# Kernel optimization log

Hardware: AMD Instinct MI355X
Metric: run time of the kernel (lower is better)

Reference implementation:

```python
import jax, jax.numpy as jnp
from jax import lax
import numpy as np

B, T, U, V = 4, 300, 64, 1024
FEAT, H, L = 80, 512, 3            # encoder: 3-layer bidirectional LSTM
HD = 512                           # decoder hidden (1 layer)
ENC_OUT = DEC_OUT = 512
INNER = 512
DMAX = max(FEAT, 2 * H)            # padded input dim for stacked encoder weights
NEG = -1e30


def setup_inputs() -> dict:
    key = jax.random.key(0)
    ks = jax.random.split(key, 20)
    s = 1.0 / np.sqrt(H)
    u = lambda k, shp: jax.random.uniform(k, shp, jnp.float32, -s, s)
    inputs = jax.random.normal(ks[0], (B, T, FEAT), jnp.float32)
    inputs_length = jax.random.randint(ks[1], (B,), T // 2, T + 1, jnp.int32)
    targets = jax.random.randint(ks[2], (B, U), 1, V, jnp.int32)
    targets_length = jax.random.randint(ks[3], (B,), U // 2, U + 1, jnp.int32)
    enc_Wih = u(ks[4], (L, 2, 4 * H, DMAX))   # layer0 uses first FEAT cols
    enc_Whh = u(ks[5], (L, 2, 4 * H, H))
    enc_b = u(ks[6], (L, 2, 4 * H))           # b_ih + b_hh fused
    enc_proj_W = u(ks[7], (ENC_OUT, 2 * H))
    enc_proj_b = u(ks[8], (ENC_OUT,))
    dec_emb = u(ks[9], (V, HD)).at[0].set(0.0)  # padding_idx=0
    dec_Wih = u(ks[10], (4 * HD, HD))
    dec_Whh = u(ks[11], (4 * HD, HD))
    dec_b = u(ks[12], (4 * HD,))
    dec_proj_W = u(ks[13], (DEC_OUT, HD))
    dec_proj_b = u(ks[14], (DEC_OUT,))
    j_fwd_W = u(ks[15], (INNER, ENC_OUT + DEC_OUT))
    j_fwd_b = u(ks[16], (INNER,))
    j_proj_W = u(ks[17], (V, INNER))
    j_proj_b = u(ks[18], (V,))
    return dict(inputs=inputs, inputs_length=inputs_length, targets=targets,
                targets_length=targets_length, enc_Wih=enc_Wih, enc_Whh=enc_Whh,
                enc_b=enc_b, enc_proj_W=enc_proj_W, enc_proj_b=enc_proj_b,
                dec_emb=dec_emb, dec_Wih=dec_Wih, dec_Whh=dec_Whh, dec_b=dec_b,
                dec_proj_W=dec_proj_W, dec_proj_b=dec_proj_b, j_fwd_W=j_fwd_W,
                j_fwd_b=j_fwd_b, j_proj_W=j_proj_W, j_proj_b=j_proj_b)


def lstm_layer(x, Wih, Whh, b):
    # x: [B, T, Din]; torch gate order (i, f, g, o)
    Bb = x.shape[0]
    Hh = Whh.shape[1]
    xg = jnp.einsum('btd,gd->btg', x, Wih) + b  # precompute input projections

    def step(carry, xt):
        h, c = carry
        g = xt + h @ Whh.T
        i, f, gg, o = jnp.split(g, 4, axis=-1)
        c = jax.nn.sigmoid(f) * c + jax.nn.sigmoid(i) * jnp.tanh(gg)
        h = jax.nn.sigmoid(o) * jnp.tanh(c)
        return (h, c), h

    z = jnp.zeros((Bb, Hh), x.dtype)
    _, hs = lax.scan(step, (z, z), xg.transpose(1, 0, 2))
    return hs.transpose(1, 0, 2)


def reverse_padded(x, lengths):
    # reverse each sequence within its valid length (packed-sequence semantics)
    t = jnp.arange(x.shape[1])
    idx = jnp.where(t[None] < lengths[:, None], lengths[:, None] - 1 - t[None], t[None])
    return jnp.take_along_axis(x, idx[:, :, None], axis=1)


def rnnt_loss(log_probs, targets, T_len, U_len):
    # log_probs: [B, T, U+1, V], blank = 0
    Bb, Tt, U1, _ = log_probs.shape
    Uu = U1 - 1
    blank = log_probs[..., 0]                                   # [B,T,U+1]
    idx = jnp.broadcast_to(targets[:, None, :, None], (Bb, Tt, Uu, 1))
    lab = jnp.take_along_axis(log_probs[:, :, :Uu, :], idx, axis=3)[..., 0]  # [B,T,U]

    def row_update(a, c):
        # solves x[u] = logaddexp(a[u], x[u-1] + c[u-1]) via log-space cumsum
        C = jnp.concatenate([jnp.zeros((Bb, 1), a.dtype), jnp.cumsum(c, axis=1)], axis=1)
        return C + lax.cumlogsumexp(a - C, axis=1)

    a0 = jnp.full((Bb, U1), NEG, log_probs.dtype).at[:, 0].set(0.0)
    alpha0 = row_update(a0, lab[:, 0])

    def step(alpha_prev, xs):
        bl_prev, lab_t = xs
        alpha = row_update(alpha_prev + bl_prev, lab_t)
        return alpha, alpha

    xs = (blank[:, :-1].transpose(1, 0, 2), lab[:, 1:].transpose(1, 0, 2))
    _, alphas = lax.scan(step, alpha0, xs)                      # [T-1,B,U+1]
    alphas = jnp.concatenate([alpha0[None], alphas], axis=0)    # [T,B,U+1]
    b_idx = jnp.arange(Bb)
    ll = alphas[T_len - 1, b_idx, U_len] + blank[b_idx, T_len - 1, U_len]
    return -jnp.mean(ll)


def reference(inputs, inputs_length, targets, targets_length, enc_Wih, enc_Whh,
              enc_b, enc_proj_W, enc_proj_b, dec_emb, dec_Wih, dec_Whh, dec_b,
              dec_proj_W, dec_proj_b, j_fwd_W, j_fwd_b, j_proj_W, j_proj_b):
    # ---- encoder: stacked bi-LSTM + projection ----
    mask = (jnp.arange(T)[None] < inputs_length[:, None])[..., None].astype(inputs.dtype)
    x = inputs
    for l in range(L):
        Din = x.shape[-1]
        fwd = lstm_layer(x, enc_Wih[l, 0, :, :Din], enc_Whh[l, 0], enc_b[l, 0])
        bwd = reverse_padded(
            lstm_layer(reverse_padded(x, inputs_length), enc_Wih[l, 1, :, :Din],
                       enc_Whh[l, 1], enc_b[l, 1]), inputs_length)
        x = jnp.concatenate([fwd, bwd], axis=-1) * mask
    enc = jnp.einsum('bth,oh->bto', x, enc_proj_W) + enc_proj_b  # [B,T,ENC_OUT]

    # ---- decoder: blank-prepended targets -> embed -> LSTM -> projection ----
    dec_in = jnp.pad(targets, ((0, 0), (1, 0)))                  # [B,U+1]
    demb = dec_emb[dec_in]
    dmask = (jnp.arange(U + 1)[None] < (targets_length + 1)[:, None])[..., None].astype(demb.dtype)
    dh = lstm_layer(demb, dec_Wih, dec_Whh, dec_b) * dmask
    dec = jnp.einsum('buh,oh->buo', dh, dec_proj_W) + dec_proj_b  # [B,U+1,DEC_OUT]

    # ---- joint: broadcast T x (U+1), split concat-matmul into two matmuls ----
    We, Wd = j_fwd_W[:, :ENC_OUT], j_fwd_W[:, ENC_OUT:]
    hj = jnp.tanh(jnp.einsum('bto,io->bti', enc, We)[:, :, None, :]
                  + jnp.einsum('buo,io->bui', dec, Wd)[:, None, :, :] + j_fwd_b)
    logits = jnp.einsum('btui,vi->btuv', hj, j_proj_W) + j_proj_b  # [B,T,U+1,V]
    log_probs = jax.nn.log_softmax(logits, axis=-1)

    return rnnt_loss(log_probs, targets, inputs_length, targets_length)
```

## Files before the change

kernel.cpp:

```cpp
#include <hip/hip_runtime.h>
#include <hip/hip_bf16.h>

#define B_ 4
#define T_ 300
#define U_ 64
#define U1_ 65
#define V_ 1024
#define H_ 512
#define G4_ 2048
#define NW_ 32
#define RPB_ (T_ * U1_)
#define NTILE_ 305
#define RPAD_ 19520
#define FASTK_ 128

typedef __hip_bfloat16 bf16;
typedef unsigned long long u64;
typedef __attribute__((ext_vector_type(8))) short short8;
typedef __attribute__((ext_vector_type(4))) float floatx4;
typedef __attribute__((ext_vector_type(4))) unsigned int uintx4;

__device__ __forceinline__ float b2f(bf16 x) { return __bfloat162float(x); }
__device__ __forceinline__ bf16 f2b(float x) { return __float2bfloat16(x); }
__device__ __forceinline__ short bf16bits(float x) {
  bf16 h = __float2bfloat16(x);
  return *reinterpret_cast<short*>(&h);
}
__device__ __forceinline__ short8 pack8(float4 a, float4 b) {
  short8 p;
  p[0] = bf16bits(a.x); p[1] = bf16bits(a.y); p[2] = bf16bits(a.z); p[3] = bf16bits(a.w);
  p[4] = bf16bits(b.x); p[5] = bf16bits(b.y); p[6] = bf16bits(b.z); p[7] = bf16bits(b.w);
  return p;
}
__device__ __forceinline__ float sigm_(float x) { return 1.f / (1.f + __expf(-x)); }
__device__ __forceinline__ float tanh_(float x) { return 1.f - 2.f / (1.f + __expf(2.f * x)); }
__device__ __forceinline__ float lae_(float x, float y) {
  float m = fmaxf(x, y);
  float n = fminf(x, y);
  return m + __logf(1.f + __expf(n - m));
}

__device__ __forceinline__ void poll4x4(const u64* a0, bool slow,
                                        uintx4& q0, uintx4& q1,
                                        uintx4& q2, uintx4& q3) {
  const u64* a1 = a0 + 512;
  const u64* a2 = a0 + 1024;
  const u64* a3 = a0 + 1536;
  if (!slow) {
    asm volatile(
        "global_load_dwordx4 %0, %4, off sc0\n\t"
        "global_load_dwordx4 %1, %5, off sc0\n\t"
        "global_load_dwordx4 %2, %6, off sc0\n\t"
        "global_load_dwordx4 %3, %7, off sc0\n\t"
        "s_waitcnt vmcnt(0)"
        : "=&v"(q0), "=&v"(q1), "=&v"(q2), "=&v"(q3)
        : "v"(a0), "v"(a1), "v"(a2), "v"(a3)
        : "memory");
  } else {
    asm volatile(
        "global_load_dwordx4 %0, %4, off sc0 sc1\n\t"
        "global_load_dwordx4 %1, %5, off sc0 sc1\n\t"
        "global_load_dwordx4 %2, %6, off sc0 sc1\n\t"
        "global_load_dwordx4 %3, %7, off sc0 sc1\n\t"
        "s_waitcnt vmcnt(0)"
        : "=&v"(q0), "=&v"(q1), "=&v"(q2), "=&v"(q3)
        : "v"(a0), "v"(a1), "v"(a2), "v"(a3)
        : "memory");
  }
}

__global__ void zero_hpk_kernel(u64* __restrict__ a, u64* __restrict__ b) {
  int i = blockIdx.x * 256 + threadIdx.x;
  if (i < 7 * 4096) { a[i] = 0ull; b[i] = 0ull; }
}

__global__ void prep_kernel(const float* __restrict__ in, bf16* __restrict__ x0) {
  int i = blockIdx.x * 256 + threadIdx.x;
  if (i < B_ * T_ * 128) {
    int k = i & 127;
    int row = i >> 7;
    float v = (k < 80) ? in[row * 80 + k] : 0.f;
    x0[(size_t)row * 1024 + k] = f2b(v);
  }
}

__global__ void embed_kernel(const float* __restrict__ emb, const int* __restrict__ tgt,
                             bf16* __restrict__ demb) {
  int i = blockIdx.x * 256 + threadIdx.x;
  if (i >= B_ * U1_ * 512) return;
  int k = i & 511;
  int bu = i >> 9;
  int u = bu % U1_, b = bu / U1_;
  int id = (u == 0) ? 0 : tgt[b * U_ + u - 1];
  demb[i] = f2b(emb[(size_t)id * 512 + k]);
}

__global__ __launch_bounds__(256) void gemm_kernel(
    const bf16* __restrict__ A, int lda,
    const float* __restrict__ W, int ldw,
    const float* __restrict__ bias,
    void* __restrict__ Cout, int out_f32, int ldc,
    int M, int K) {
  __shared__ __align__(16) bf16 As[64][72];
  __shared__ __align__(16) bf16 Bs[64][72];
  int m0 = blockIdx.x * 64, n0 = blockIdx.y * 64;
  int tid = threadIdx.x, w = tid >> 6, l = tid & 63;
  int l4 = l & 15, lq = l >> 4;
  floatx4 acc[4];
#pragma unroll
  for (int nt = 0; nt < 4; ++nt) acc[nt] = (floatx4){0.f, 0.f, 0.f, 0.f};
  for (int k0 = 0; k0 < K; k0 += 64) {
    __syncthreads();
#pragma unroll
    for (int q = 0; q < 2; ++q) {
      int cc = tid + q * 256;
      int r = cc >> 3, kc = (cc & 7) * 8;
      short8 va = {0, 0, 0, 0, 0, 0, 0, 0};
      int gm = m0 + r;
      if (gm < M) va = *(const short8*)(A + (size_t)gm * lda + k0 + kc);
      *(short8*)(&As[r][kc]) = va;
      const float* wp = W + (size_t)(n0 + r) * ldw + k0 + kc;
      float4 w0 = *(const float4*)(wp);
      float4 w1 = *(const float4*)(wp + 4);
      *(short8*)(&Bs[r][kc]) = pack8(w0, w1);
    }
    __syncthreads();
#pragma unroll
    for (int kk = 0; kk < 64; kk += 32) {
      short8 a = *(const short8*)(&As[w * 16 + l4][kk + lq * 8]);
#pragma unroll
      for (int nt = 0; nt < 4; ++nt) {
        short8 bb = *(const short8*)(&Bs[nt * 16 + l4][kk + lq * 8]);
        acc[nt] = __builtin_amdgcn_mfma_f32_16x16x32_bf16(a, bb, acc[nt], 0, 0, 0);
      }
    }
  }
#pragma unroll
  for (int nt = 0; nt < 4; ++nt) {
    int col = n0 + nt * 16 + l4;
    float bv = bias ? bias[col] : 0.f;
#pragma unroll
    for (int r = 0; r < 4; ++r) {
      int row = m0 + w * 16 + lq * 4 + r;
      if (row < M) {
        float v = acc[nt][r] + bv;
        if (out_f32) ((float*)Cout)[(size_t)row * ldc + col] = v;
        else ((bf16*)Cout)[(size_t)row * ldc + col] = f2b(v);
      }
    }
  }
}

__global__ __launch_bounds__(256, 1) void scan_kernel(
    int ndir,
    const float* __restrict__ xg,
    const float* __restrict__ whh,
    const int* __restrict__ len_raw, int len_add,
    int Tmax, int bwd_mask,
    bf16* __restrict__ out, int out_stride,
    int dec_d,
    const float* __restrict__ xg2, const float* __restrict__ whh2,
    const int* __restrict__ len_raw2, int len_add2,
    int Tmax2, bf16* __restrict__ out2, int out_stride2,
    u64* __restrict__ hpkS, u64* __restrict__ hpkF) {
  int d = blockIdx.x, w = blockIdx.y;
  if (d >= ndir) return;
  int tid = threadIdx.x;
  bool isdec = (d == dec_d);
  const float* xg_d = isdec ? xg2 : xg + (size_t)d * B_ * Tmax * G4_;
  const float* whh_d = isdec ? whh2 : whh + (size_t)d * G4_ * H_;
  const int* lens = isdec ? len_raw2 : len_raw;
  int ladd = isdec ? len_add2 : len_add;
  int tmax = isdec ? Tmax2 : Tmax;
  bf16* outp = isdec ? out2 : out;
  int ostride = isdec ? out_stride2 : out_stride;
  int ocol = isdec ? 0 : d * H_;
  bool bwd = isdec ? false : ((bwd_mask >> d) & 1);
  u64* hpS = hpkS + (size_t)d * 4096;
  u64* hpF = hpkF + (size_t)d * 4096;

  int sub = tid >> 6;
  int l = tid & 63;
  int col = l & 15;
  int lq = l >> 4;
  int gate = col & 3;
  int dloc = col >> 2;
  int dim = w * 16 + sub * 4 + dloc;
  int grow = gate * H_ + dim;
  int sb = l & 12;

  __shared__ int len_s[4];
  __shared__ __align__(16) bf16 h_lds[2][16][512];

  if (tid < 4) len_s[tid] = lens[tid] + ladd;
  {
    unsigned* hz = (unsigned*)&h_lds[0][0][0];
#pragma unroll
    for (int i = 0; i < 32; ++i) hz[tid + i * 256] = 0u;
  }

  short8 bfr[16];
  {
    const float* wp = whh_d + (size_t)grow * H_ + lq * 8;
#pragma unroll
    for (int ks2 = 0; ks2 < 16; ++ks2) {
      float4 w0 = *(const float4*)(wp + ks2 * 32);
      float4 w1 = *(const float4*)(wp + ks2 * 32 + 4);
      bfr[ks2] = pack8(w0, w1);
    }
  }
  __syncthreads();
  int smax = max(max(len_s[0], len_s[1]), max(len_s[2], len_s[3]));

  int D0 = sub * 128 + 2 * l;
  float cst = 0.f;
  char* hbase = (char*)&h_lds[0][0][0];
  unsigned rsw = (unsigned)((l & 7) << 4);
  unsigned rbyte = (unsigned)((l & 15) * 1024 + lq * 16);

  bool slowp = false;

  float xv[4];
  if (l < 16) {
#pragma unroll
    for (int b = 0; b < 4; ++b) {
      int lb = len_s[b];
      int rt = bwd ? (lb - 1) : 0;
      xv[b] = xg_d[((size_t)b * tmax + rt) * G4_ + grow];
    }
  }

  for (int s = 0; s < smax; ++s) {
    int p = s & 1;
    char* pl = hbase + p * 16384;
    if (s > 0) {
      unsigned ss = (unsigned)s;
      const u64* srcS = hpS + ((s - 1) & 1) * 2048 + D0;
      const u64* srcF = hpF + ((s - 1) & 1) * 2048 + D0;
      uintx4 q0, q1, q2, q3;
      int it = 0;
      for (;;) {
        poll4x4(slowp ? srcS : srcF, slowp, q0, q1, q2, q3);
        bool ok = (q0[0] == ss) & (q0[2] == ss) & (q1[0] == ss) & (q1[2] == ss) &
                  (q2[0] == ss) & (q2[2] == ss) & (q3[0] == ss) & (q3[2] == ss);
        if (__all(ok)) break;
        if (!slowp && ++it > FASTK_) slowp = true;
      }
      unsigned cb = (unsigned)(D0 * 2);
      unsigned pay0[4] = {q0[1], q1[1], q2[1], q3[1]};
      unsigned pay1[4] = {q0[3], q1[3], q2[3], q3[3]};
#pragma unroll
      for (int b = 0; b < 4; ++b) {
        float f0 = __uint_as_float(pay0[b]);
        float f1 = __uint_as_float(pay1[b]);
        bf16 h0 = f2b(f0), h1 = f2b(f1);
        float r0 = f0 - b2f(h0), r1 = f1 - b2f(h1);
        bf16 e0 = f2b(r0), e1 = f2b(r1);
        unsigned hi = (unsigned)*(unsigned short*)&h0 |
                      ((unsigned)*(unsigned short*)&h1 << 16);
        unsigned lo = (unsigned)*(unsigned short*)&e0 |
                      ((unsigned)*(unsigned short*)&e1 << 16);
        *(unsigned*)(pl + (((unsigned)(b * 1024) + cb) ^ (unsigned)(b << 4))) = hi;
        *(unsigned*)(pl + (((unsigned)((b + 4) * 1024) + cb) ^ (unsigned)((b + 4) << 4))) = lo;
      }
    }
    float xvn[4];
    if (l < 16) {
      int sn = s + 1;
#pragma unroll
      for (int b = 0; b < 4; ++b) {
        int lb = len_s[b];
        int rt = bwd ? (lb - 1 - sn) : sn;
        if (sn >= lb) rt = 0;
        xvn[b] = xg_d[((size_t)b * tmax + rt) * G4_ + grow];
      }
    }
    __syncthreads();
    floatx4 accA = (floatx4){0.f, 0.f, 0.f, 0.f};
    floatx4 accB = (floatx4){0.f, 0.f, 0.f, 0.f};
#pragma unroll
    for (int k2 = 0; k2 < 16; k2 += 2) {
      short8 a0 = *(const short8*)(pl + ((rbyte + (unsigned)(k2 * 64)) ^ rsw));
      short8 a1 = *(const short8*)(pl + ((rbyte + (unsigned)((k2 + 1) * 64)) ^ rsw));
      accA = __builtin_amdgcn_mfma_f32_16x16x32_bf16(a0, bfr[k2], accA, 0, 0, 0);
      accB = __builtin_amdgcn_mfma_f32_16x16x32_bf16(a1, bfr[k2 + 1], accB, 0, 0, 0);
    }
    floatx4 acc = accA + accB;
    float hout = 0.f;
#pragma unroll
    for (int r = 0; r < 4; ++r) {
      float v2 = acc[r] + __shfl(acc[r], col + 16, 64);
      if (l < 16) v2 += xv[r];
      float gi = __shfl(v2, sb + 0, 64);
      float gf = __shfl(v2, sb + 1, 64);
      float gg = __shfl(v2, sb + 2, 64);
      float go = __shfl(v2, sb + 3, 64);
      if (l < 16 && (l & 3) == r && s < len_s[r]) {
        cst = sigm_(gf) * cst + sigm_(gi) * tanh_(gg);
        hout = sigm_(go) * tanh_(cst);
      }
    }
    if (l < 16) {
      int b = l & 3;
      u64 pkt = ((u64)__float_as_uint(hout) << 32) | (unsigned)(s + 1);
      u64* paF = hpF + p * 2048 + b * 512 + dim;
      u64* paS = hpS + p * 2048 + b * 512 + dim;
      asm volatile("global_store_dwordx2 %0, %1, off sc0" ::"v"(paF), "v"(pkt)
                   : "memory");
      asm volatile("global_store_dwordx2 %0, %1, off sc0 sc1" ::"v"(paS), "v"(pkt)
                   : "memory");
      if (s < len_s[b]) {
        int t = bwd ? (len_s[b] - 1 - s) : s;
        outp[((size_t)b * tmax + t) * ostride + ocol + dim] = f2b(hout);
      }
    }
#pragma unroll
    for (int b = 0; b < 4; ++b) xv[b] = xvn[b];
  }
}

__global__ __launch_bounds__(256) void joint_kernel(
    const float* __restrict__ ea, const float* __restrict__ da,
    const float* __restrict__ Wp, const float* __restrict__ pb,
    const int* __restrict__ targets,
    float* __restrict__ blankraw, float* __restrict__ labraw,
    float* __restrict__ jstats) {
  __shared__ __align__(16) bf16 As[64][72];
  __shared__ __align__(16) bf16 Bs[256][72];
  __shared__ float bias_s[256];
  __shared__ int tgt_s[64];
  __shared__ float pstat[64][2][2];

  int tid = threadIdx.x;
  int tile = blockIdx.x, cb = blockIdx.y, b = blockIdx.z;
  int r0 = tile * 64;

  bias_s[tid & 255] = pb[cb * 256 + (tid & 255)];
  if (tid < 64) {
    int r = r0 + tid;
    int u = r % U1_;
    tgt_s[tid] = (r < RPB_ && u < U_) ? targets[b * U_ + u] : -1;
  }
  int si = tid >> 2;
  int sseg = (tid & 3) * 16;
  int sr = r0 + si;
  bool svalid = sr < RPB_;
  int st = svalid ? sr / U1_ : 0;
  int su = svalid ? sr % U1_ : 0;
  const float* ep = ea + ((size_t)(b * T_ + st)) * 512 + sseg;
  const float* dp = da + ((size_t)(b * U1_ + su)) * 512 + sseg;

  int wid = tid >> 6, l = tid & 63;
  int wm = wid >> 1, wn = wid & 1;
  int l4 = l & 15, lq = l >> 4;

  floatx4 acc[2][8];
#pragma unroll
  for (int ms = 0; ms < 2; ++ms)
#pragma unroll
    for (int nt = 0; nt < 8; ++nt) acc[ms][nt] = (floatx4){0.f, 0.f, 0.f, 0.f};

  for (int k0 = 0; k0 < 512; k0 += 64) {
    __syncthreads();
    {
      const float* e = ep + k0;
      const float* d = dp + k0;
#pragma unroll
      for (int h = 0; h < 2; ++h) {
        float4 e0 = *(const float4*)(e + h * 8);
        float4 e1 = *(const float4*)(e + h * 8 + 4);
        float4 d0 = *(const float4*)(d + h * 8);
        float4 d1 = *(const float4*)(d + h * 8 + 4);
        short8 pk = {0, 0, 0, 0, 0, 0, 0, 0};
        if (svalid) {
          pk[0] = bf16bits(tanh_(e0.x + d0.x));
          pk[1] = bf16bits(tanh_(e0.y + d0.y));
          pk[2] = bf16bits(tanh_(e0.z + d0.z));
          pk[3] = bf16bits(tanh_(e0.w + d0.w));
          pk[4] = bf16bits(tanh_(e1.x + d1.x));
          pk[5] = bf16bits(tanh_(e1.y + d1.y));
          pk[6] = bf16bits(tanh_(e1.z + d1.z));
          pk[7] = bf16bits(tanh_(e1.w + d1.w));
        }
        *(short8*)(&As[si][sseg + h * 8]) = pk;
      }
    }
#pragma unroll
    for (int q = 0; q < 8; ++q) {
      int cc = tid + q * 256;
      int r = cc >> 3, kc = (cc & 7) * 8;
      const float* wp = Wp + (size_t)(cb * 256 + r) * 512 + k0 + kc;
      float4 w0 = *(const float4*)(wp);
      float4 w1 = *(const float4*)(wp + 4);
      *(short8*)(&Bs[r][kc]) = pack8(w0, w1);
    }
    __syncthreads();
#pragma unroll
    for (int kk = 0; kk < 64; kk += 32) {
      short8 af[2], bf8[8];
#pragma unroll
      for (int ms = 0; ms < 2; ++ms)
        af[ms] = *(const short8*)(&As[wm * 32 + ms * 16 + l4][kk + lq * 8]);
#pragma unroll
      for (int nt = 0; nt < 8; ++nt)
        bf8[nt] = *(const short8*)(&Bs[wn * 128 + nt * 16 + l4][kk + lq * 8]);
#pragma unroll
      for (int ms = 0; ms < 2; ++ms)
#pragma unroll
        for (int nt = 0; nt < 8; ++nt)
          acc[ms][nt] = __builtin_amdgcn_mfma_f32_16x16x32_bf16(af[ms], bf8[nt], acc[ms][nt], 0, 0, 0);
    }
  }
#pragma unroll
  for (int ms = 0; ms < 2; ++ms) {
#pragma unroll
    for (int r = 0; r < 4; ++r) {
      int i = wm * 32 + ms * 16 + lq * 4 + r;
      int grow = r0 + i;
      bool valid = grow < RPB_;
      int tg = tgt_s[i];
      float v[8];
      float mx = -1e30f;
#pragma unroll
      for (int nt = 0; nt < 8; ++nt) {
        int colc = wn * 128 + nt * 16 + l4;
        float x = acc[ms][nt][r] + bias_s[colc];
        v[nt] = x;
        mx = fmaxf(mx, x);
        int gcol = cb * 256 + colc;
        if (valid) {
          if (gcol == 0) blankraw[(size_t)b * RPB_ + grow] = x;
          if (gcol == tg) labraw[(size_t)b * RPB_ + grow] = x;
        }
      }
#pragma unroll
      for (int dd = 1; dd < 16; dd <<= 1) mx = fmaxf(mx, __shfl_xor(mx, dd, 64));
      float se = 0.f;
#pragma unroll
      for (int nt = 0; nt < 8; ++nt) se += __expf(v[nt] - mx);
#pragma unroll
      for (int dd = 1; dd < 16; dd <<= 1) se += __shfl_xor(se, dd, 64);
      if (l4 == 0) { pstat[i][wn][0] = mx; pstat[i][wn][1] = se; }
    }
  }
  __syncthreads();
  if (tid < 64) {
    float ma = pstat[tid][0][0], sa = pstat[tid][0][1];
    float mb = pstat[tid][1][0], sb = pstat[tid][1][1];
    float mc = fmaxf(ma, mb);
    float sc = sa * __expf(ma - mc) + sb * __expf(mb - mc);
    size_t o = (((size_t)b * RPAD_ + r0 + tid) * 4 + cb) * 2;
    jstats[o] = mc;
    jstats[o + 1] = sc;
  }
}

__global__ void finalize_kernel(const float* __restrict__ jstats,
                                float* __restrict__ blank, float* __restrict__ lab) {
  int g = blockIdx.x * 256 + threadIdx.x;
  if (g >= B_ * RPB_) return;
  int b = g / RPB_, r = g % RPB_;
  const float* st = jstats + ((size_t)b * RPAD_ + r) * 8;
  float M = fmaxf(fmaxf(st[0], st[2]), fmaxf(st[4], st[6]));
  float s = st[1] * __expf(st[0] - M) + st[3] * __expf(st[2] - M) +
            st[5] * __expf(st[4] - M) + st[7] * __expf(st[6] - M);
  float lse = M + __logf(s);
  blank[g] -= lse;
  if ((r % U1_) < U_) lab[g] -= lse;
}

__global__ void loss_kernel(const float* __restrict__ blank, const float* __restrict__ lab,
                            const int* __restrict__ Tl, const int* __restrict__ Ul,
                            float* __restrict__ outp) {
  int b = threadIdx.x >> 6;
  int l = threadIdx.x & 63;
  int TL = Tl[b], UL = Ul[b];
  float alpha_l = 0.f, alpha0 = 0.f;
  for (int t = 0; t < TL; ++t) {
    float a_u0, a_l1;
    if (t == 0) { a_u0 = 0.f; a_l1 = -1e30f; }
    else {
      const float* bl = blank + ((size_t)b * T_ + (t - 1)) * U1_;
      a_u0 = alpha0 + bl[0];
      a_l1 = alpha_l + bl[l + 1];
    }
    const float* lb = lab + ((size_t)b * T_ + t) * U1_;
    float C = lb[l];
#pragma unroll
    for (int dd = 1; dd < 64; dd <<= 1) {
      float o = __shfl_up(C, dd, 64);
      if (l >= dd) C += o;
    }
    float S = a_l1 - C;
#pragma unroll
    for (int dd = 1; dd < 64; dd <<= 1) {
      float o = __shfl_up(S, dd, 64);
      if (l >= dd) S = lae_(S, o);
    }
    alpha_l = C + lae_(a_u0, S);
    alpha0 = a_u0;
  }
  float av = (UL == 0) ? alpha0 : __shfl(alpha_l, UL - 1, 64);
  float ll = av + blank[((size_t)b * T_ + (TL - 1)) * U1_ + UL];
  __shared__ float lls[4];
  if (l == 0) lls[b] = ll;
  __syncthreads();
  if (threadIdx.x == 0) outp[0] = -0.25f * (lls[0] + lls[1] + lls[2] + lls[3]);
}

static constexpr size_t OFF_XG = 0;
static constexpr size_t OFF_XA = OFF_XG + (size_t)2 * B_ * T_ * G4_ * 4;
static constexpr size_t OFF_XB = OFF_XA + (size_t)B_ * T_ * 1024 * 2;
static constexpr size_t OFF_ENC = OFF_XB + (size_t)B_ * T_ * 1024 * 2;
static constexpr size_t OFF_EA = OFF_ENC + (size_t)B_ * T_ * 512 * 2;
static constexpr size_t OFF_DEMB = OFF_EA + (size_t)B_ * T_ * 512 * 4;
static constexpr size_t OFF_DXG = OFF_DEMB + (size_t)B_ * U1_ * 512 * 2;
static constexpr size_t OFF_DH = OFF_DXG + (size_t)B_ * U1_ * G4_ * 4;
static constexpr size_t OFF_DEC = OFF_DH + (size_t)B_ * U1_ * 512 * 2;
static constexpr size_t OFF_DA = OFF_DEC + (size_t)B_ * U1_ * 512 * 2;
static constexpr size_t OFF_BL = OFF_DA + (size_t)B_ * U1_ * 512 * 4;
static constexpr size_t OFF_LAB = OFF_BL + (size_t)B_ * T_ * U1_ * 4;
static constexpr size_t OFF_HPK = OFF_LAB + (size_t)B_ * T_ * U1_ * 4;
static constexpr size_t OFF_JST = OFF_HPK + (size_t)7 * 4096 * 8;
static constexpr size_t OFF_FPK = OFF_JST + (size_t)B_ * RPAD_ * 4 * 2 * 4;

extern "C" void kernel_launch(void* const* d_in, const int* in_sizes, int n_in,
                              void* d_out, int out_size, void* d_ws, size_t ws_size,
                              hipStream_t stream) {
  (void)in_sizes; (void)n_in; (void)out_size; (void)ws_size;
  const float* inputs = (const float*)d_in[0];
  const int* inputs_length = (const int*)d_in[1];
  const int* targets = (const int*)d_in[2];
  const int* targets_length = (const int*)d_in[3];
  const float* enc_Wih = (const float*)d_in[4];
  const float* enc_Whh = (const float*)d_in[5];
  const float* enc_b = (const float*)d_in[6];
  const float* enc_proj_W = (const float*)d_in[7];
  const float* enc_proj_b = (const float*)d_in[8];
  const float* dec_emb = (const float*)d_in[9];
  const float* dec_Wih = (const float*)d_in[10];
  const float* dec_Whh = (const float*)d_in[11];
  const float* dec_b = (const float*)d_in[12];
  const float* dec_proj_W = (const float*)d_in[13];
  const float* dec_proj_b = (const float*)d_in[14];
  const float* j_fwd_W = (const float*)d_in[15];
  const float* j_fwd_b = (const float*)d_in[16];
  const float* j_proj_W = (const float*)d_in[17];
  const float* j_proj_b = (const float*)d_in[18];

  char* ws = (char*)d_ws;
  float* xg = (float*)(ws + OFF_XG);
  bf16* xa = (bf16*)(ws + OFF_XA);
  bf16* xb = (bf16*)(ws + OFF_XB);
  bf16* encb = (bf16*)(ws + OFF_ENC);
  float* eab = (float*)(ws + OFF_EA);
  bf16* demb = (bf16*)(ws + OFF_DEMB);
  float* dxg = (float*)(ws + OFF_DXG);
  bf16* dh = (bf16*)(ws + OFF_DH);
  bf16* decb = (bf16*)(ws + OFF_DEC);
  float* dab = (float*)(ws + OFF_DA);
  float* blank = (float*)(ws + OFF_BL);
  float* lab = (float*)(ws + OFF_LAB);
  u64* hpkS = (u64*)(ws + OFF_HPK);
  u64* hpkF = (u64*)(ws + OFF_FPK);
  float* jstats = (float*)(ws + OFF_JST);

  zero_hpk_kernel<<<112, 256, 0, stream>>>(hpkS, hpkF);
  prep_kernel<<<600, 256, 0, stream>>>(inputs, xa);
  embed_kernel<<<520, 256, 0, stream>>>(dec_emb, targets, demb);

  gemm_kernel<<<dim3(5, 32), 256, 0, stream>>>(demb, 512, dec_Wih, 512, dec_b,
                                               dxg, 1, G4_, B_ * U1_, 512);
  for (int dd = 0; dd < 2; ++dd) {
    gemm_kernel<<<dim3(19, 32), 256, 0, stream>>>(
        xa, 1024, enc_Wih + (size_t)dd * G4_ * 1024, 1024, enc_b + (size_t)dd * G4_,
        xg + (size_t)dd * B_ * T_ * G4_, 1, G4_, B_ * T_, 128);
  }
  scan_kernel<<<dim3(8, NW_), 256, 0, stream>>>(
      3, xg, enc_Whh, inputs_length, 0, T_, 2, xb, 1024,
      2, dxg, dec_Whh, targets_length, 1, U1_, dh, 512,
      hpkS, hpkF);

  gemm_kernel<<<dim3(5, 8), 256, 0, stream>>>(dh, 512, dec_proj_W, 512, dec_proj_b,
                                              decb, 0, 512, B_ * U1_, 512);
  gemm_kernel<<<dim3(5, 8), 256, 0, stream>>>(decb, 512, j_fwd_W + 512, 1024, j_fwd_b,
                                              dab, 1, 512, B_ * U1_, 512);

  bf16* xcur = xb;
  for (int lyr = 1; lyr < 3; ++lyr) {
    bf16* xnext = (xcur == xa) ? xb : xa;
    for (int dd = 0; dd < 2; ++dd) {
      gemm_kernel<<<dim3(19, 32), 256, 0, stream>>>(
          xcur, 1024,
          enc_Wih + (size_t)(lyr * 2 + dd) * G4_ * 1024, 1024,
          enc_b + (size_t)(lyr * 2 + dd) * G4_,
          xg + (size_t)dd * B_ * T_ * G4_, 1, G4_, B_ * T_, 1024);
    }
    scan_kernel<<<dim3(8, NW_), 256, 0, stream>>>(
        2, xg, enc_Whh + (size_t)lyr * 2 * G4_ * H_,
        inputs_length, 0, T_, 2, xnext, 1024,
        -1, dxg, dec_Whh, targets_length, 1, U1_, dh, 512,
        hpkS + (size_t)(3 + 2 * (lyr - 1)) * 4096,
        hpkF + (size_t)(3 + 2 * (lyr - 1)) * 4096);
    xcur = xnext;
  }
  gemm_kernel<<<dim3(19, 8), 256, 0, stream>>>(xcur, 1024, enc_proj_W, 1024, enc_proj_b,
                                               encb, 0, 512, B_ * T_, 1024);
  gemm_kernel<<<dim3(19, 8), 256, 0, stream>>>(encb, 512, j_fwd_W, 1024, (const float*)nullptr,
                                               eab, 1, 512, B_ * T_, 512);

  joint_kernel<<<dim3(NTILE_, 4, B_), 256, 0, stream>>>(eab, dab, j_proj_W, j_proj_b, targets,
                                                        blank, lab, jstats);
  finalize_kernel<<<(B_ * RPB_ + 255) / 256, 256, 0, stream>>>(jstats, blank, lab);
  loss_kernel<<<1, 256, 0, stream>>>(blank, lab, inputs_length, targets_length, (float*)d_out);
}
```

Measured before the change: 3.539 ms.

## Issue next-step h polls early in LSTM recurrence to overlap flag latency

Splits the flag-polling helper so the four global loads for the next step's hidden-state packets are issued right after publishing this step's output, before the output store and next xg load. At the top of the next step it waits with a partial vmcnt and checks readiness, falling back to the old re-poll loop only if flags are stale. The xg prefetch is moved into the step itself. The intent is to hide the round-trip latency of cross-workgroup synchronization, at the cost of a possibly wasted early poll and extra s_waitcnt(0) after stores.

```diff
diff --git a/kernel.cpp b/kernel.cpp
--- a/kernel.cpp
+++ b/kernel.cpp
@@ -40,9 +40,9 @@
   return m + __logf(1.f + __expf(n - m));
 }
 
-__device__ __forceinline__ void poll4x4(const u64* a0, bool slow,
-                                        uintx4& q0, uintx4& q1,
-                                        uintx4& q2, uintx4& q3) {
+__device__ __forceinline__ void issue_polls(const u64* a0, bool slow,
+                                            uintx4& q0, uintx4& q1,
+                                            uintx4& q2, uintx4& q3) {
   const u64* a1 = a0 + 512;
   const u64* a2 = a0 + 1024;
   const u64* a3 = a0 + 1536;
@@ -51,8 +51,7 @@
         "global_load_dwordx4 %0, %4, off sc0\n\t"
         "global_load_dwordx4 %1, %5, off sc0\n\t"
         "global_load_dwordx4 %2, %6, off sc0\n\t"
-        "global_load_dwordx4 %3, %7, off sc0\n\t"
-        "s_waitcnt vmcnt(0)"
+        "global_load_dwordx4 %3, %7, off sc0"
         : "=&v"(q0), "=&v"(q1), "=&v"(q2), "=&v"(q3)
         : "v"(a0), "v"(a1), "v"(a2), "v"(a3)
         : "memory");
@@ -61,8 +60,7 @@
         "global_load_dwordx4 %0, %4, off sc0 sc1\n\t"
         "global_load_dwordx4 %1, %5, off sc0 sc1\n\t"
         "global_load_dwordx4 %2, %6, off sc0 sc1\n\t"
-        "global_load_dwordx4 %3, %7, off sc0 sc1\n\t"
-        "s_waitcnt vmcnt(0)"
+        "global_load_dwordx4 %3, %7, off sc0 sc1"
         : "=&v"(q0), "=&v"(q1), "=&v"(q2), "=&v"(q3)
         : "v"(a0), "v"(a1), "v"(a2), "v"(a3)
         : "memory");
@@ -219,32 +217,43 @@
   unsigned rbyte = (unsigned)((l & 15) * 1024 + lq * 16);
 
   bool slowp = false;
-
-  float xv[4];
-  if (l < 16) {
-#pragma unroll
-    for (int b = 0; b < 4; ++b) {
-      int lb = len_s[b];
-      int rt = bwd ? (lb - 1) : 0;
-      xv[b] = xg_d[((size_t)b * tmax + rt) * G4_ + grow];
-    }
-  }
+  uintx4 q0 = {0, 0, 0, 0}, q1 = {0, 0, 0, 0}, q2 = {0, 0, 0, 0}, q3 = {0, 0, 0, 0};
+
+#define WAITVM(N)                                                        \
+  do {                                                                   \
+    asm volatile("s_waitcnt vmcnt(" #N ")"                               \
+                 : "+v"(q0), "+v"(q1), "+v"(q2), "+v"(q3)::"memory");    \
+    __builtin_amdgcn_sched_barrier(0);                                   \
+  } while (0)
+#define CHKOK()                                                          \
+  ((q0[0] == ss) & (q0[2] == ss) & (q1[0] == ss) & (q1[2] == ss) &       \
+   (q2[0] == ss) & (q2[2] == ss) & (q3[0] == ss) & (q3[2] == ss))
 
   for (int s = 0; s < smax; ++s) {
     int p = s & 1;
     char* pl = hbase + p * 16384;
+    float xv[4];
+    if (l < 16) {
+#pragma unroll
+      for (int b = 0; b < 4; ++b) {
+        int lb = len_s[b];
+        int rt = bwd ? (lb - 1 - s) : s;
+        if (s >= lb) rt = 0;
+        xv[b] = xg_d[((size_t)b * tmax + rt) * G4_ + grow];
+      }
+    }
     if (s > 0) {
       unsigned ss = (unsigned)s;
-      const u64* srcS = hpS + ((s - 1) & 1) * 2048 + D0;
-      const u64* srcF = hpF + ((s - 1) & 1) * 2048 + D0;
-      uintx4 q0, q1, q2, q3;
+      WAITVM(5);
+      bool ok = CHKOK();
       int it = 0;
-      for (;;) {
-        poll4x4(slowp ? srcS : srcF, slowp, q0, q1, q2, q3);
-        bool ok = (q0[0] == ss) & (q0[2] == ss) & (q1[0] == ss) & (q1[2] == ss) &
-                  (q2[0] == ss) & (q2[2] == ss) & (q3[0] == ss) & (q3[2] == ss);
-        if (__all(ok)) break;
+      while (!__all(ok)) {
+        WAITVM(0);
         if (!slowp && ++it > FASTK_) slowp = true;
+        const u64* src = (slowp ? hpS : hpF) + ((s - 1) & 1) * 2048 + D0;
+        issue_polls(src, slowp, q0, q1, q2, q3);
+        WAITVM(0);
+        ok = CHKOK();
       }
       unsigned cb = (unsigned)(D0 * 2);
       unsigned pay0[4] = {q0[1], q1[1], q2[1], q3[1]};
@@ -264,17 +273,6 @@
         *(unsigned*)(pl + (((unsigned)((b + 4) * 1024) + cb) ^ (unsigned)((b + 4) << 4))) = lo;
       }
     }
-    float xvn[4];
-    if (l < 16) {
-      int sn = s + 1;
-#pragma unroll
-      for (int b = 0; b < 4; ++b) {
-        int lb = len_s[b];
-        int rt = bwd ? (lb - 1 - sn) : sn;
-        if (sn >= lb) rt = 0;
-        xvn[b] = xg_d[((size_t)b * tmax + rt) * G4_ + grow];
-      }
-    }
     __syncthreads();
     floatx4 accA = (floatx4){0.f, 0.f, 0.f, 0.f};
     floatx4 accB = (floatx4){0.f, 0.f, 0.f, 0.f};
@@ -309,14 +307,22 @@
                    : "memory");
       asm volatile("global_store_dwordx2 %0, %1, off sc0 sc1" ::"v"(paS), "v"(pkt)
                    : "memory");
+    }
+    asm volatile("s_waitcnt vmcnt(0)" ::: "memory");
+    {
+      const u64* nsrc = (slowp ? hpS : hpF) + p * 2048 + D0;
+      issue_polls(nsrc, slowp, q0, q1, q2, q3);
+    }
+    if (l < 16) {
+      int b = l & 3;
       if (s < len_s[b]) {
         int t = bwd ? (len_s[b] - 1 - s) : s;
         outp[((size_t)b * tmax + t) * ostride + ocol + dim] = f2b(hout);
       }
     }
-#pragma unroll
-    for (int b = 0; b < 4; ++b) xv[b] = xvn[b];
-  }
+  }
+#undef WAITVM
+#undef CHKOK
 }
 
 __global__ __launch_bounds__(256) void joint_kernel(
```

After: 4.056 ms. 14.6% more time.
